# Kernel optimization log

Hardware: AMD Instinct MI355X
Metric: run time of the kernel (lower is better)

## Reference

```python
import jax, jax.numpy as jnp
import numpy as np

H = 512; L = 2; V = 128; B = 128; T = 256; LW = 32; SOS = 1


def _lstm_scan(xs, Wih, Whh, b, reverse=False):
    # xs: [B, T, in]; Wih: [in, 4H]; Whh: [H, 4H]; b: [4H]
    Bq, Hh = xs.shape[0], Whh.shape[0]
    h0 = jnp.zeros((Bq, Hh), xs.dtype)

    def step(carry, xt):
        h, c = carry
        i, f, g, o = jnp.split(xt @ Wih + h @ Whh + b, 4, axis=-1)
        c = jax.nn.sigmoid(f) * c + jax.nn.sigmoid(i) * jnp.tanh(g)
        h = jax.nn.sigmoid(o) * jnp.tanh(c)
        return (h, c), h

    (hT, cT), ys = jax.lax.scan(step, (h0, h0), jnp.swapaxes(xs, 0, 1), reverse=reverse)
    return jnp.swapaxes(ys, 0, 1), hT, cT


def setup_inputs() -> dict:
    key = jax.random.key(0)
    ks = jax.random.split(key, 17)
    s = 0.05
    rn = lambda k, shape: jax.random.normal(k, shape, jnp.float32) * s
    return {
        'x': jax.random.normal(ks[0], (B, T, 2), jnp.float32),
        'enc_l0_Wih': rn(ks[1], (2, 2, 4 * H)),
        'enc_l0_Whh': rn(ks[2], (2, H, 4 * H)),
        'enc_l0_b': rn(ks[3], (2, 4 * H)),
        'enc_l1_Wih': rn(ks[4], (2, 2 * H, 4 * H)),
        'enc_l1_Whh': rn(ks[5], (2, H, 4 * H)),
        'enc_l1_b': rn(ks[6], (2, 4 * H)),
        'dec_Wih': rn(ks[7], (L, H, 4 * H)),
        'dec_Whh': rn(ks[8], (L, H, 4 * H)),
        'dec_b': rn(ks[9], (L, 4 * H)),
        'emb': rn(ks[10], (V, H)),
        'Wq': rn(ks[11], (H, 2 * H)),
        'bq': rn(ks[12], (2 * H,)),
        'Wc': rn(ks[13], (3 * H, H)),
        'bc': rn(ks[14], (H,)),
        'Wf': rn(ks[15], (H, V)),
        'bf': rn(ks[16], (V,)),
    }


def _forward(x, enc_l0_Wih, enc_l0_Whh, enc_l0_b, enc_l1_Wih, enc_l1_Whh, enc_l1_b,
             dec_Wih, dec_Whh, dec_b, emb, Wq, bq, Wc, bc, Wf, bf):
    # --- encoder: 2-layer bidirectional LSTM ---
    hs, cs = [], []
    inp = x
    for (Wih, Whh, b) in ((enc_l0_Wih, enc_l0_Whh, enc_l0_b),
                          (enc_l1_Wih, enc_l1_Whh, enc_l1_b)):
        yf, hf, cf = _lstm_scan(inp, Wih[0], Whh[0], b[0], reverse=False)
        yb, hb, cb = _lstm_scan(inp, Wih[1], Whh[1], b[1], reverse=True)
        inp = jnp.concatenate([yf, yb], axis=-1)
        hs.append(hf + hb)  # sum fwd+bwd final states (as in original)
        cs.append(cf + cb)
    enc_outs = inp                     # [B, T, 2H]
    h0 = jnp.stack(hs)                 # [L, B, H]
    c0 = jnp.stack(cs)
    tok0 = jnp.full((x.shape[0],), SOS, jnp.int32)

    def dec_step(carry, _):
        h, c, tok = carry
        layer_in = emb[tok]            # [B, H]
        nh, nc = [], []
        for l in range(L):
            i, f, g, o = jnp.split(layer_in @ dec_Wih[l] + h[l] @ dec_Whh[l] + dec_b[l], 4, axis=-1)
            cl = jax.nn.sigmoid(f) * c[l] + jax.nn.sigmoid(i) * jnp.tanh(g)
            hl = jax.nn.sigmoid(o) * jnp.tanh(cl)
            nh.append(hl); nc.append(cl)
            layer_in = hl
        dec_out = layer_in             # [B, H]
        query = dec_out @ Wq + bq      # [B, 2H]
        attn = jax.nn.softmax(jnp.einsum('bte,be->bt', enc_outs, query), axis=1)  # [B, T]
        context = jnp.einsum('bt,bte->be', attn, enc_outs)                        # [B, 2H]
        combined = jnp.concatenate([dec_out, context], axis=-1) @ Wc + bc         # [B, H]
        logits = combined @ Wf + bf                                                # [B, V]
        tok = jnp.argmax(logits, axis=-1).astype(jnp.int32)
        return (jnp.stack(nh), jnp.stack(nc), tok), (logits, attn)

    (hF, cF, _), (logits_seq, attn_seq) = jax.lax.scan(dec_step, (h0, c0, tok0), None, length=LW)
    output_seq = jnp.swapaxes(logits_seq, 0, 1)        # [B, LW, V]
    attention = jnp.transpose(attn_seq, (1, 2, 0))     # [B, T, LW]
    return output_seq, hF, cF, attention


def reference(x, enc_l0_Wih, enc_l0_Whh, enc_l0_b, enc_l1_Wih, enc_l1_Whh, enc_l1_b,
              dec_Wih, dec_Whh, dec_b, emb, Wq, bq, Wc, bc, Wf, bf):
    return _forward(x, enc_l0_Wih, enc_l0_Whh, enc_l0_b, enc_l1_Wih, enc_l1_Whh, enc_l1_b,
                    dec_Wih, dec_Whh, dec_b, emb, Wq, bq, Wc, bc, Wf, bf)
```

## Files before the change

### kernel.cpp

```cpp
#include <hip/hip_runtime.h>
#include <hip/hip_fp16.h>
#include <hip/hip_cooperative_groups.h>
#include <math.h>

#define NB 128
#define NT 256
#define NH 512
#define NG 2048
#define NV 128
#define NLW 32

__device__ __forceinline__ float sigf(float x){ return 1.0f/(1.0f + expf(-x)); }
__device__ __forceinline__ void fma4(float4& a, float s, float4 w){
  a.x += s*w.x; a.y += s*w.y; a.z += s*w.z; a.w += s*w.w;
}
__device__ __forceinline__ float4 ldh4(const __half* p){
  const __half2* p2 = (const __half2*)p;
  const float2 a = __half22float2(p2[0]);
  const float2 b = __half22float2(p2[1]);
  return make_float4(a.x, a.y, b.x, b.y);
}
__device__ __forceinline__ void ldh8(const __half* p, float4& lo, float4& hi){
  const float4 raw = *(const float4*)p;
  const __half2* h2 = (const __half2*)&raw;
  const float2 a = __half22float2(h2[0]);
  const float2 b = __half22float2(h2[1]);
  const float2 c = __half22float2(h2[2]);
  const float2 d = __half22float2(h2[3]);
  lo = make_float4(a.x, a.y, b.x, b.y);
  hi = make_float4(c.x, c.y, d.x, d.y);
}
__device__ __forceinline__ void dot4(float& acc, const float4 a, const float4 b){
  acc += a.x*b.x + a.y*b.y + a.z*b.z + a.w*b.w;
}

__device__ __forceinline__ void stc_f(float* p, float v){
  union { float f; unsigned u; } c; c.f = v;
  __hip_atomic_store((unsigned*)p, c.u, __ATOMIC_RELAXED, __HIP_MEMORY_SCOPE_AGENT);
}
__device__ __forceinline__ void stc_i(int* p, int v){
  __hip_atomic_store(p, v, __ATOMIC_RELAXED, __HIP_MEMORY_SCOPE_AGENT);
}

#define BAR_FLAG0 1088
#define BAR_INTS  (1088 + 256*32)

__device__ __forceinline__ void bar_core(int* bar, int step) {
  const int g = blockIdx.x >> 4;
  const int prev = __hip_atomic_fetch_add(&bar[g*64], 1,
                     __ATOMIC_RELAXED, __HIP_MEMORY_SCOPE_AGENT);
  if (prev == 15) {
    const int r = __hip_atomic_fetch_add(&bar[16*64], 1,
                     __ATOMIC_RELAXED, __HIP_MEMORY_SCOPE_AGENT);
    if (r == 15) {
      #pragma unroll
      for (int i = 0; i < 16; ++i)
        __hip_atomic_store(&bar[i*64], 0, __ATOMIC_RELAXED, __HIP_MEMORY_SCOPE_AGENT);
      __hip_atomic_store(&bar[16*64], 0, __ATOMIC_RELAXED, __HIP_MEMORY_SCOPE_AGENT);
      asm volatile("s_waitcnt vmcnt(0)" ::: "memory");
      #pragma unroll 8
      for (int i = 0; i < 256; ++i)
        __hip_atomic_store(&bar[BAR_FLAG0 + i*32], step,
                           __ATOMIC_RELAXED, __HIP_MEMORY_SCOPE_AGENT);
    }
  }
}
__device__ __forceinline__ void grid_arrive(int* bar, int step) {
  __syncthreads();
  if (threadIdx.x == 0) {
    asm volatile("s_waitcnt vmcnt(0)" ::: "memory");
    bar_core(bar, step);
  }
}
__device__ __forceinline__ void grid_arrive_f(int* bar, int step) {
  __syncthreads();
  if (threadIdx.x == 0) {
    __threadfence();
    bar_core(bar, step);
  }
}
__device__ __forceinline__ void grid_wait(int* bar, int step) {
  if (threadIdx.x == 0) {
    int* my = &bar[BAR_FLAG0 + blockIdx.x*32];
    while (__hip_atomic_load(my, __ATOMIC_RELAXED,
                             __HIP_MEMORY_SCOPE_AGENT) < step)
      __builtin_amdgcn_s_sleep(2);
    __threadfence();
  }
  __syncthreads();
}

struct EncParams {
  const float* x;
  const float* W0ih; const float* W0hh; const float* b0;
  const float* W1ih; const float* W1hh; const float* b1;
  __half* y0; __half* enc;
  float* h0buf; float* h1buf;
  float* c0fin; float* c1fin;
  int*   bar;
};

#define W1T_ROW 1542
#define W0T_ROW 518
#define ENC_LDS_FLOATS (16*W1T_ROW + 16*W0T_ROW + 16 + 16 + 128*17)
#define ENC_LDS_BYTES  (ENC_LDS_FLOATS*4)

__device__ __forceinline__ void l1_ih_part(const __half* y0t, const float* W1T,
                                           const float* bias1, int bg2, int cg2,
                                           float acc[2][4]) {
  #pragma unroll
  for (int i = 0; i < 2; ++i)
    #pragma unroll
    for (int j = 0; j < 4; ++j)
      acc[i][j] = bias1[cg2*4 + j];
  const long r0 = (long)(bg2*2+0)*1024, r1 = (long)(bg2*2+1)*1024;
  #pragma unroll 2
  for (int k = 0; k < 1024; k += 8) {
    float4 a0lo, a0hi, a1lo, a1hi;
    ldh8(y0t + r0 + k, a0lo, a0hi);
    ldh8(y0t + r1 + k, a1lo, a1hi);
    #pragma unroll
    for (int j = 0; j < 4; ++j) {
      const float4 wlo = *(const float4*)&W1T[(cg2*4+j)*W1T_ROW + k];
      const float4 whi = *(const float4*)&W1T[(cg2*4+j)*W1T_ROW + k + 4];
      dot4(acc[0][j], a0lo, wlo); dot4(acc[0][j], a0hi, whi);
      dot4(acc[1][j], a1lo, wlo); dot4(acc[1][j], a1hi, whi);
    }
  }
}

__global__ __launch_bounds__(256, 1)
void encoder_kernel(EncParams P) {
  const int tid = threadIdx.x;
  const int bid = blockIdx.x;
  const int dir = bid >> 7;
  const int n0  = (bid & 127) * 4;
  int* bar = P.bar;

  extern __shared__ float lds[];
  float* W1T   = lds;
  float* W0T   = lds + 16*W1T_ROW;
  float* bias0 = W0T + 16*W0T_ROW;
  float* bias1 = bias0 + 16;
  float* gsm   = bias1 + 16;

  {
    const float* Wih1 = P.W1ih + (long)dir*1024*NG;
    const float* Whh1 = P.W1hh + (long)dir*512*NG;
    for (int e = tid; e < 16*1536; e += 256) {
      const int ci = e & 15, kk = e >> 4;
      const int gc = (ci>>2)*NH + n0 + (ci&3);
      W1T[ci*W1T_ROW + kk] = (kk < 1024) ? Wih1[(long)kk*NG + gc]
                                         : Whh1[(long)(kk-1024)*NG + gc];
    }
    const float* Wih0 = P.W0ih + (long)dir*2*NG;
    const float* Whh0 = P.W0hh + (long)dir*512*NG;
    for (int e = tid; e < 16*512; e += 256) {
      const int ci = e & 15, kk = e >> 4;
      const int gc = (ci>>2)*NH + n0 + (ci&3);
      W0T[ci*W0T_ROW + 4 + kk] = Whh0[(long)kk*NG + gc];
    }
    if (tid < 32) {
      const int ci = tid & 15, kk = tid >> 4;
      const int gc = (ci>>2)*NH + n0 + (ci&3);
      W0T[ci*W0T_ROW + kk] = Wih0[(long)kk*NG + gc];
    }
    if (tid < 16) {
      const int gc = (tid>>2)*NH + n0 + (tid&3);
      bias0[tid] = P.b0[(long)dir*NG + gc];
      bias1[tid] = P.b1[(long)dir*NG + gc];
    }
  }
  __syncthreads();

  int gstep = 0;
  float creg0 = 0.f, creg1 = 0.f;

  {
    const int bg1 = tid >> 3;
    const int cg1 = tid & 7;
    for (int p = 0; p < NT; ++p) {
      const int t = dir ? (NT-1 - p) : p;
      const float* hp = P.h0buf + (long)((p&1)*2 + dir)*65536;
      float acc[4][2];
      #pragma unroll
      for (int i = 0; i < 4; ++i) { acc[i][0] = bias0[cg1*2]; acc[i][1] = bias0[cg1*2+1]; }
      {
        const float w00 = W0T[(cg1*2+0)*W0T_ROW + 0], w01 = W0T[(cg1*2+0)*W0T_ROW + 1];
        const float w10 = W0T[(cg1*2+1)*W0T_ROW + 0], w11 = W0T[(cg1*2+1)*W0T_ROW + 1];
        #pragma unroll
        for (int i = 0; i < 4; ++i) {
          const int b = bg1*4 + i;
          const float x0 = P.x[(long)b*(NT*2) + t*2 + 0];
          const float x1 = P.x[(long)b*(NT*2) + t*2 + 1];
          acc[i][0] += x0*w00 + x1*w01;
          acc[i][1] += x0*w10 + x1*w11;
        }
      }
      #pragma unroll 4
      for (int k = 0; k < NH; k += 4) {
        const float4 w0 = *(const float4*)&W0T[(cg1*2+0)*W0T_ROW + 4 + k];
        const float4 w1 = *(const float4*)&W0T[(cg1*2+1)*W0T_ROW + 4 + k];
        #pragma unroll
        for (int i = 0; i < 4; ++i) {
          const float4 a = *(const float4*)&hp[(long)(bg1*4+i)*NH + k];
          dot4(acc[i][0], a, w0);
          dot4(acc[i][1], a, w1);
        }
      }
      #pragma unroll
      for (int i = 0; i < 4; ++i) {
        gsm[(bg1*4+i)*17 + cg1*2 + 0] = acc[i][0];
        gsm[(bg1*4+i)*17 + cg1*2 + 1] = acc[i][1];
      }
      __syncthreads();
      {
        float* hnext = P.h0buf + (long)(((p+1)&1)*2 + dir)*65536;
        #pragma unroll
        for (int r = 0; r < 2; ++r) {
          const int pi2 = tid + r*256;
          const int b = pi2 >> 2, nl = pi2 & 3;
          const float iv = gsm[b*17 + 0  + nl];
          const float fv = gsm[b*17 + 4  + nl];
          const float gv = gsm[b*17 + 8  + nl];
          const float ov = gsm[b*17 + 12 + nl];
          float cold = r ? creg1 : creg0;
          const float cn = sigf(fv)*cold + sigf(iv)*tanhf(gv);
          const float hn = sigf(ov)*tanhf(cn);
          if (r) creg1 = cn; else creg0 = cn;
          stc_f(&hnext[(long)b*NH + n0 + nl], hn);
          P.y0[((long)t*NB + b)*1024 + dir*NH + n0 + nl] = __float2half_rn(hn);
        }
      }
      ++gstep;
      if (p < NT-1) grid_arrive(bar, gstep);
      else          grid_arrive_f(bar, gstep);
      grid_wait(bar, gstep);
    }
    #pragma unroll
    for (int r = 0; r < 2; ++r) {
      const int pi2 = tid + r*256;
      P.c0fin[(long)dir*65536 + (long)(pi2>>2)*NH + n0 + (pi2&3)] = r ? creg1 : creg0;
    }
    creg0 = 0.f; creg1 = 0.f;
  }

  {
    const int bg2 = tid >> 2;
    const int cg2 = tid & 3;
    float accN[2][4], accC[2][4];
    {
      const int t0i = dir ? (NT-1) : 0;
      l1_ih_part(P.y0 + (long)t0i*NB*1024, W1T, bias1, bg2, cg2, accN);
    }
    for (int p = 0; p < NT; ++p) {
      const int t = dir ? (NT-1 - p) : p;
      #pragma unroll
      for (int i = 0; i < 2; ++i)
        #pragma unroll
        for (int j = 0; j < 4; ++j)
          accC[i][j] = accN[i][j];
      {
        const float* hp = P.h1buf + (long)((p&1)*2 + dir)*65536;
        const long r0 = (long)(bg2*2+0)*NH, r1 = (long)(bg2*2+1)*NH;
        #pragma unroll 4
        for (int k = 0; k < NH; k += 4) {
          const float4 w0 = *(const float4*)&W1T[(cg2*4+0)*W1T_ROW + 1024 + k];
          const float4 w1 = *(const float4*)&W1T[(cg2*4+1)*W1T_ROW + 1024 + k];
          const float4 w2 = *(const float4*)&W1T[(cg2*4+2)*W1T_ROW + 1024 + k];
          const float4 w3 = *(const float4*)&W1T[(cg2*4+3)*W1T_ROW + 1024 + k];
          const float4 a0 = *(const float4*)&hp[r0 + k];
          const float4 a1 = *(const float4*)&hp[r1 + k];
          dot4(accC[0][0], a0, w0); dot4(accC[0][1], a0, w1);
          dot4(accC[0][2], a0, w2); dot4(accC[0][3], a0, w3);
          dot4(accC[1][0], a1, w0); dot4(accC[1][1], a1, w1);
          dot4(accC[1][2], a1, w2); dot4(accC[1][3], a1, w3);
        }
      }
      #pragma unroll
      for (int i = 0; i < 2; ++i)
        #pragma unroll
        for (int j = 0; j < 4; ++j)
          gsm[(bg2*2+i)*17 + cg2*4 + j] = accC[i][j];
      __syncthreads();
      {
        float* hnext = P.h1buf + (long)(((p+1)&1)*2 + dir)*65536;
        #pragma unroll
        for (int r = 0; r < 2; ++r) {
          const int pi2 = tid + r*256;
          const int b = pi2 >> 2, nl = pi2 & 3;
          const float iv = gsm[b*17 + 0  + nl];
          const float fv = gsm[b*17 + 4  + nl];
          const float gv = gsm[b*17 + 8  + nl];
          const float ov = gsm[b*17 + 12 + nl];
          float cold = r ? creg1 : creg0;
          const float cn = sigf(fv)*cold + sigf(iv)*tanhf(gv);
          const float hn = sigf(ov)*tanhf(cn);
          if (r) creg1 = cn; else creg0 = cn;
          stc_f(&hnext[(long)b*NH + n0 + nl], hn);
          P.enc[((long)t*NB + b)*1024 + dir*NH + n0 + nl] = __float2half_rn(hn);
        }
      }
      if (p < NT-1) {
        ++gstep; grid_arrive(bar, gstep);
        const int tn = dir ? (NT-1 - (p+1)) : (p+1);
        l1_ih_part(P.y0 + (long)tn*NB*1024, W1T, bias1, bg2, cg2, accN);
        grid_wait(bar, gstep);
      }
    }
    #pragma unroll
    for (int r = 0; r < 2; ++r) {
      const int pi2 = tid + r*256;
      P.c1fin[(long)dir*65536 + (long)(pi2>>2)*NH + n0 + (pi2&3)] = r ? creg1 : creg0;
    }
  }
}

struct DecParams {
  const float* emb;
  const float* dWih; const float* dWhh; const float* dbv;
  const float* Wq;  const float* bq;
  const float* Wc;  const float* bc;
  const float* Wf;  const float* bf;
  const __half* enc;
  const float* h0e; const float* h1e;
  const float* c0fin; const float* c1fin;
  float* dh0; float* dh1;
  float* query; float* ctx; float* comb;
  int*   tok;
  float* dout;
  int*   bar;
};

#define WD_ROW 1026
#define WQ_ROW 514
#define WC_ROW 1538
#define DEC_LDS_FLOATS (16*WD_ROW + 4*WQ_ROW + 2*WC_ROW + 16 + 4 + 2 + 128*17 \
                        + 1024 + 256 + 64 + 4 + 512 + 128 + 128)
#define DEC_LDS_BYTES  (DEC_LDS_FLOATS*4)

__global__ __launch_bounds__(256, 1)
void decoder_kernel(DecParams P) {
  const int tid = threadIdx.x;
  const int lid = blockIdx.x;
  const int L   = lid >> 7;
  const int n0  = (lid & 127) * 4;
  const int qc0 = lid * 4;
  const int cc0 = lid * 2;
  int* bar = P.bar;

  extern __shared__ float lds[];
  float* WD    = lds;
  float* WqT   = WD + 16*WD_ROW;
  float* WcT   = WqT + 4*WQ_ROW;
  float* biasD = WcT + 2*WC_ROW;
  float* bq4   = biasD + 16;
  float* bc2   = bq4 + 4;
  float* gsm   = bc2 + 2;
  float* qs    = gsm + 128*17;
  float* sc    = qs + 1024;
  float* ps    = sc + 256;
  float* m3    = ps + 64;
  float* cs    = m3 + 4;
  float* vals  = cs + 512;
  int*   idxs  = (int*)(vals + 128);

  {
    const float* Wih = P.dWih + (long)L*512*NG;
    const float* Whh = P.dWhh + (long)L*512*NG;
    for (int e = tid; e < 16*1024; e += 256) {
      const int ci = e & 15, kk = e >> 4;
      const int gc = (ci>>2)*NH + n0 + (ci&3);
      WD[ci*WD_ROW + kk] = (kk < 512) ? Wih[(long)kk*NG + gc]
                                      : Whh[(long)(kk-512)*NG + gc];
    }
    for (int e = tid; e < 4*512; e += 256) {
      const int c = e & 3, kk = e >> 2;
      WqT[c*WQ_ROW + kk] = P.Wq[(long)kk*1024 + qc0 + c];
    }
    for (int e = tid; e < 2*1536; e += 256) {
      const int c = e & 1, kk = e >> 1;
      WcT[c*WC_ROW + kk] = P.Wc[(long)kk*NH + cc0 + c];
    }
    if (tid < 16) biasD[tid] = P.dbv[(long)L*NG + (tid>>2)*NH + n0 + (tid&3)];
    if (tid < 4)  bq4[tid] = P.bq[qc0 + tid];
    if (tid < 2)  bc2[tid] = P.bc[cc0 + tid];
    const int i = lid*256 + tid;
    stc_f(&P.dh0[i], P.h0e[i] + P.h0e[65536 + i]);
    stc_f(&P.dh1[i], P.h1e[i] + P.h1e[65536 + i]);
    if (i < NB) stc_i(&P.tok[i], 1);
  }
  float cregA, cregB;
  {
    const float* cf = L ? P.c1fin : P.c0fin;
    const int b0i = tid >> 2, nl0 = tid & 3;
    cregA = cf[(long)b0i*NH + n0 + nl0] + cf[65536 + (long)b0i*NH + n0 + nl0];
    const int pi2 = tid + 256;
    const int b1i = pi2 >> 2, nl1 = pi2 & 3;
    cregB = cf[(long)b1i*NH + n0 + nl1] + cf[65536 + (long)b1i*NH + n0 + nl1];
  }
  int gstep = 0;
  ++gstep; grid_arrive(bar, gstep); grid_wait(bar, gstep);

  const int bg = tid >> 3;
  const int cg = tid & 7;

  for (int s = 0; s < NLW; ++s) {
    float* dh0c = P.dh0 + (s&1)*65536;
    float* dh0n = P.dh0 + ((s+1)&1)*65536;
    float* dh1c = P.dh1 + (s&1)*65536;
    float* dh1n = P.dh1 + ((s+1)&1)*65536;

    if (L == 0) {
      float acc[4][2];
      #pragma unroll
      for (int i = 0; i < 4; ++i) { acc[i][0] = biasD[cg*2]; acc[i][1] = biasD[cg*2+1]; }
      int rows[4];
      #pragma unroll
      for (int i = 0; i < 4; ++i) rows[i] = P.tok[bg*4 + i];
      #pragma unroll 4
      for (int k = 0; k < NH; k += 4) {
        const float4 w0 = *(const float4*)&WD[(cg*2+0)*WD_ROW + k];
        const float4 w1 = *(const float4*)&WD[(cg*2+1)*WD_ROW + k];
        #pragma unroll
        for (int i = 0; i < 4; ++i) {
          const float4 a = *(const float4*)&P.emb[(long)rows[i]*NH + k];
          dot4(acc[i][0], a, w0);
          dot4(acc[i][1], a, w1);
        }
      }
      #pragma unroll 4
      for (int k = 0; k < NH; k += 4) {
        const float4 w0 = *(const float4*)&WD[(cg*2+0)*WD_ROW + 512 + k];
        const float4 w1 = *(const float4*)&WD[(cg*2+1)*WD_ROW + 512 + k];
        #pragma unroll
        for (int i = 0; i < 4; ++i) {
          const float4 a = *(const float4*)&dh0c[(long)(bg*4+i)*NH + k];
          dot4(acc[i][0], a, w0);
          dot4(acc[i][1], a, w1);
        }
      }
      #pragma unroll
      for (int i = 0; i < 4; ++i) {
        gsm[(bg*4+i)*17 + cg*2 + 0] = acc[i][0];
        gsm[(bg*4+i)*17 + cg*2 + 1] = acc[i][1];
      }
      __syncthreads();
      #pragma unroll
      for (int r = 0; r < 2; ++r) {
        const int pi2 = tid + r*256;
        const int b = pi2 >> 2, nl = pi2 & 3;
        const float iv = gsm[b*17 + 0  + nl];
        const float fv = gsm[b*17 + 4  + nl];
        const float gv = gsm[b*17 + 8  + nl];
        const float ov = gsm[b*17 + 12 + nl];
        const float cold = r ? cregB : cregA;
        const float cn = sigf(fv)*cold + sigf(iv)*tanhf(gv);
        const float hn = sigf(ov)*tanhf(cn);
        if (r) cregB = cn; else cregA = cn;
        stc_f(&dh0n[(long)b*NH + n0 + nl], hn);
      }
    }
    ++gstep; grid_arrive(bar, gstep); grid_wait(bar, gstep);

    if (L == 1) {
      float acc[4][2];
      #pragma unroll
      for (int i = 0; i < 4; ++i) { acc[i][0] = biasD[cg*2]; acc[i][1] = biasD[cg*2+1]; }
      #pragma unroll 4
      for (int k = 0; k < NH; k += 4) {
        const float4 w0 = *(const float4*)&WD[(cg*2+0)*WD_ROW + k];
        const float4 w1 = *(const float4*)&WD[(cg*2+1)*WD_ROW + k];
        #pragma unroll
        for (int i = 0; i < 4; ++i) {
          const float4 a = *(const float4*)&dh0n[(long)(bg*4+i)*NH + k];
          dot4(acc[i][0], a, w0);
          dot4(acc[i][1], a, w1);
        }
      }
      #pragma unroll 4
      for (int k = 0; k < NH; k += 4) {
        const float4 w0 = *(const float4*)&WD[(cg*2+0)*WD_ROW + 512 + k];
        const float4 w1 = *(const float4*)&WD[(cg*2+1)*WD_ROW + 512 + k];
        #pragma unroll
        for (int i = 0; i < 4; ++i) {
          const float4 a = *(const float4*)&dh1c[(long)(bg*4+i)*NH + k];
          dot4(acc[i][0], a, w0);
          dot4(acc[i][1], a, w1);
        }
      }
      #pragma unroll
      for (int i = 0; i < 4; ++i) {
        gsm[(bg*4+i)*17 + cg*2 + 0] = acc[i][0];
        gsm[(bg*4+i)*17 + cg*2 + 1] = acc[i][1];
      }
      __syncthreads();
      #pragma unroll
      for (int r = 0; r < 2; ++r) {
        const int pi2 = tid + r*256;
        const int b = pi2 >> 2, nl = pi2 & 3;
        const float iv = gsm[b*17 + 0  + nl];
        const float fv = gsm[b*17 + 4  + nl];
        const float gv = gsm[b*17 + 8  + nl];
        const float ov = gsm[b*17 + 12 + nl];
        const float cold = r ? cregB : cregA;
        const float cn = sigf(fv)*cold + sigf(iv)*tanhf(gv);
        const float hn = sigf(ov)*tanhf(cn);
        if (r) cregB = cn; else cregA = cn;
        stc_f(&dh1n[(long)b*NH + n0 + nl], hn);
      }
    }
    ++gstep; grid_arrive(bar, gstep); grid_wait(bar, gstep);

    {
      const int b = tid >> 1;
      const int ch = (tid & 1) * 2;
      float a0 = bq4[ch + 0], a1 = bq4[ch + 1];
      const float* hr = dh1n + (long)b*NH;
      #pragma unroll 4
      for (int k = 0; k < NH; k += 4) {
        const float4 a = *(const float4*)&hr[k];
        const float4 w0 = *(const float4*)&WqT[(ch+0)*WQ_ROW + k];
        const float4 w1 = *(const float4*)&WqT[(ch+1)*WQ_ROW + k];
        dot4(a0, a, w0);
        dot4(a1, a, w1);
      }
      stc_f(&P.query[(long)b*1024 + qc0 + ch + 0], a0);
      stc_f(&P.query[(long)b*1024 + qc0 + ch + 1], a1);
    }
    ++gstep; grid_arrive(bar, gstep); grid_wait(bar, gstep);

    if (lid < NB) {
      const int b = lid;
      for (int i = tid; i < 1024; i += 256) qs[i] = P.query[(long)b*1024 + i];
      if (tid == 0) { m3[0] = -1e30f; m3[1] = 0.f; m3[2] = 0.f; }
      __syncthreads();
      float4 ctx4 = {0,0,0,0};
      for (int c = 0; c < 4; ++c) {
        const int t0 = c*64;
        {
          const int t_l = tid >> 2, part = tid & 3;
          const __half* er = P.enc + ((long)(t0 + t_l)*NB + b)*1024 + part*256;
          const float* qr = qs + part*256;
          float sv = 0.f;
          for (int k = 0; k < 256; k += 4) {
            const float4 e4 = ldh4(er + k);
            const float4 q4 = *(const float4*)(qr + k);
            sv += e4.x*q4.x + e4.y*q4.y + e4.z*q4.z + e4.w*q4.w;
          }
          sv += __shfl_xor(sv, 1);
          sv += __shfl_xor(sv, 2);
          if (part == 0) sc[t0 + t_l] = sv;
        }
        __syncthreads();
        if (tid < 64) {
          float sv = sc[t0 + tid];
          for (int off = 32; off; off >>= 1) sv = fmaxf(sv, __shfl_xor(sv, off));
          if (tid == 0) {
            const float mn = fmaxf(m3[0], sv);
            m3[2] = expf(m3[0] - mn);
            m3[0] = mn;
          }
        }
        __syncthreads();
        const float alpha = m3[2];
        if (tid < 64) {
          float pv = expf(sc[t0 + tid] - m3[0]);
          ps[tid] = pv;
          for (int off = 32; off; off >>= 1) pv += __shfl_xor(pv, off);
          if (tid == 0) m3[1] = m3[1]*alpha + pv;
        }
        __syncthreads();
        ctx4.x *= alpha; ctx4.y *= alpha; ctx4.z *= alpha; ctx4.w *= alpha;
        const __half* ecol = P.enc + ((long)t0*NB + b)*1024 + tid*4;
        for (int t = 0; t < 64; ++t) {
          const float4 e4 = ldh4(ecol + (long)t*(NB*1024));
          fma4(ctx4, ps[t], e4);
        }
        __syncthreads();
      }
      const float linv = 1.0f / m3[1];
      const long cb = (long)b*1024 + tid*4;
      stc_f(&P.ctx[cb+0], ctx4.x*linv); stc_f(&P.ctx[cb+1], ctx4.y*linv);
      stc_f(&P.ctx[cb+2], ctx4.z*linv); stc_f(&P.ctx[cb+3], ctx4.w*linv);
      const float pv = expf(sc[tid] - m3[0]) * linv;
      stc_f(&P.dout[786432L + (long)b*(NT*NLW) + (long)tid*NLW + s], pv);
    }
    ++gstep; grid_arrive(bar, gstep); grid_wait(bar, gstep);

    {
      const int b = tid >> 1;
      const int col = tid & 1;
      float acc = bc2[col];
      const float* hr = dh1n + (long)b*NH;
      #pragma unroll 4
      for (int k = 0; k < NH; k += 4) {
        const float4 a = *(const float4*)&hr[k];
        const float4 w = *(const float4*)&WcT[col*WC_ROW + k];
        dot4(acc, a, w);
      }
      const float* cr = P.ctx + (long)b*1024;
      #pragma unroll 4
      for (int k = 0; k < 1024; k += 4) {
        const float4 a = *(const float4*)&cr[k];
        const float4 w = *(const float4*)&WcT[col*WC_ROW + 512 + k];
        dot4(acc, a, w);
      }
      stc_f(&P.comb[(long)b*NH + cc0 + col], acc);
    }
    ++gstep; grid_arrive(bar, gstep); grid_wait(bar, gstep);

    if (lid < NB) {
      const int b = lid;
      for (int i = tid; i < NH; i += 256) cs[i] = P.comb[(long)b*NH + i];
      __syncthreads();
      if (tid < NV) {
        float acc = P.bf[tid];
        for (int k = 0; k < NH; k += 4) {
          const float4 c4 = *(const float4*)&cs[k];
          acc += c4.x*P.Wf[(long)(k+0)*NV + tid];
          acc += c4.y*P.Wf[(long)(k+1)*NV + tid];
          acc += c4.z*P.Wf[(long)(k+2)*NV + tid];
          acc += c4.w*P.Wf[(long)(k+3)*NV + tid];
        }
        stc_f(&P.dout[(long)b*(NLW*NV) + (long)s*NV + tid], acc);
        vals[tid] = acc; idxs[tid] = tid;
      }
      __syncthreads();
      for (int st = 64; st > 0; st >>= 1) {
        if (tid < st) {
          const float v2 = vals[tid+st]; const int i2 = idxs[tid+st];
          if (v2 > vals[tid] || (v2 == vals[tid] && i2 < idxs[tid])) { vals[tid] = v2; idxs[tid] = i2; }
        }
        __syncthreads();
      }
      if (tid == 0) stc_i(&P.tok[b], idxs[0]);
    }
    ++gstep; grid_arrive(bar, gstep); grid_wait(bar, gstep);
  }

  {
    const int i = lid*256 + tid;
    P.dout[524288L + i]         = P.dh0[i];
    P.dout[524288L + 65536 + i] = P.dh1[i];
    #pragma unroll
    for (int r = 0; r < 2; ++r) {
      const int pi2 = tid + r*256;
      const int b = pi2 >> 2, nl = pi2 & 3;
      P.dout[655360L + (long)L*65536 + (long)b*NH + n0 + nl] = r ? cregB : cregA;
    }
  }
}

struct StepDir {
  const void*  A;
  const float* WA;
  const float* Bs;
  const float* WB;
  const float* x2;
  const float* Wx;
  const int*   rowIdxA;
  const float* bias;
  float*  c_io;
  float*  h_out;
  __half* yh_out;
  int sA, KA, sB, KB, sx2, ystride, aHalf;
};
struct StepParams { StepDir d[2]; };

__global__ __launch_bounds__(256)
void lstm_step_kernel(StepParams P) {
  const StepDir p = P.d[blockIdx.z];
  const int tid = threadIdx.x;
  const int nq  = tid & 3;
  const int g   = (tid >> 2) & 3;
  const int bp  = tid >> 4;
  const int bl0 = bp*2;
  const int b0  = blockIdx.y*32 + bl0;
  const int n0  = blockIdx.x*16 + nq*4;
  const int gc  = g*NH + n0;

  float4 acc0 = *(const float4*)(p.bias + gc);
  float4 acc1 = acc0;

  if (p.x2) {
    const float4 w0 = *(const float4*)(p.Wx + gc);
    const float4 w1 = *(const float4*)(p.Wx + NG + gc);
    const float* xr0 = p.x2 + (long)b0     * p.sx2;
    const float* xr1 = p.x2 + (long)(b0+1) * p.sx2;
    fma4(acc0, xr0[0], w0); fma4(acc0, xr0[1], w1);
    fma4(acc1, xr1[0], w0); fma4(acc1, xr1[1], w1);
  }
  if (p.KA > 0) {
    const int r0 = p.rowIdxA ? p.rowIdxA[b0]   : b0;
    const int r1 = p.rowIdxA ? p.rowIdxA[b0+1] : b0+1;
    const float* Wp = p.WA + gc;
    if (p.aHalf) {
      const __half* rA0 = (const __half*)p.A + (long)r0 * p.sA;
      const __half* rA1 = (const __half*)p.A + (long)r1 * p.sA;
      for (int k = 0; k < p.KA; k += 4) {
        const float4 a0 = ldh4(rA0 + k);
        const float4 a1 = ldh4(rA1 + k);
        const float4 w0 = *(const float4*)(Wp + (long)(k+0)*NG);
        const float4 w1 = *(const float4*)(Wp + (long)(k+1)*NG);
        const float4 w2 = *(const float4*)(Wp + (long)(k+2)*NG);
        const float4 w3 = *(const float4*)(Wp + (long)(k+3)*NG);
        fma4(acc0, a0.x, w0); fma4(acc0, a0.y, w1); fma4(acc0, a0.z, w2); fma4(acc0, a0.w, w3);
        fma4(acc1, a1.x, w0); fma4(acc1, a1.y, w1); fma4(acc1, a1.z, w2); fma4(acc1, a1.w, w3);
      }
    } else {
      const float* rA0 = (const float*)p.A + (long)r0 * p.sA;
      const float* rA1 = (const float*)p.A + (long)r1 * p.sA;
      for (int k = 0; k < p.KA; k += 4) {
        const float4 a0 = *(const float4*)(rA0 + k);
        const float4 a1 = *(const float4*)(rA1 + k);
        const float4 w0 = *(const float4*)(Wp + (long)(k+0)*NG);
        const float4 w1 = *(const float4*)(Wp + (long)(k+1)*NG);
        const float4 w2 = *(const float4*)(Wp + (long)(k+2)*NG);
        const float4 w3 = *(const float4*)(Wp + (long)(k+3)*NG);
        fma4(acc0, a0.x, w0); fma4(acc0, a0.y, w1); fma4(acc0, a0.z, w2); fma4(acc0, a0.w, w3);
        fma4(acc1, a1.x, w0); fma4(acc1, a1.y, w1); fma4(acc1, a1.z, w2); fma4(acc1, a1.w, w3);
      }
    }
  }
  {
    const float* rB0 = p.Bs + (long)b0     * p.sB;
    const float* rB1 = p.Bs + (long)(b0+1) * p.sB;
    const float* Wp = p.WB + gc;
    for (int k = 0; k < p.KB; k += 4) {
      const float4 a0 = *(const float4*)(rB0 + k);
      const float4 a1 = *(const float4*)(rB1 + k);
      const float4 w0 = *(const float4*)(Wp + (long)(k+0)*NG);
      const float4 w1 = *(const float4*)(Wp + (long)(k+1)*NG);
      const float4 w2 = *(const float4*)(Wp + (long)(k+2)*NG);
      const float4 w3 = *(const float4*)(Wp + (long)(k+3)*NG);
      fma4(acc0, a0.x, w0); fma4(acc0, a0.y, w1); fma4(acc0, a0.z, w2); fma4(acc0, a0.w, w3);
      fma4(acc1, a1.x, w0); fma4(acc1, a1.y, w1); fma4(acc1, a1.z, w2); fma4(acc1, a1.w, w3);
    }
  }

  __shared__ __align__(16) float gs[32][68];
  {
    float* r0 = &gs[bl0][g*17 + nq*4];
    r0[0]=acc0.x; r0[1]=acc0.y; r0[2]=acc0.z; r0[3]=acc0.w;
    float* r1 = &gs[bl0+1][g*17 + nq*4];
    r1[0]=acc1.x; r1[1]=acc1.y; r1[2]=acc1.z; r1[3]=acc1.w;
  }
  __syncthreads();
  for (int pi = tid; pi < 512; pi += 256) {
    const int b_l = pi >> 4, n_l = pi & 15;
    const float iv = gs[b_l][0*17 + n_l];
    const float fv = gs[b_l][1*17 + n_l];
    const float gv = gs[b_l][2*17 + n_l];
    const float ov = gs[b_l][3*17 + n_l];
    const int bg = blockIdx.y*32 + b_l;
    const long idx = (long)bg*NH + blockIdx.x*16 + n_l;
    const float c_old = p.c_io[idx];
    const float cn = sigf(fv)*c_old + sigf(iv)*tanhf(gv);
    const float hn = sigf(ov)*tanhf(cn);
    p.c_io[idx]  = cn;
    p.h_out[idx] = hn;
    if (p.yh_out)
      p.yh_out[(long)bg*p.ystride + blockIdx.x*16 + n_l] = __float2half_rn(hn);
  }
}

struct LinParams {
  const float* A; const float* Bs; const float* W; const float* bias;
  float* out;
  int sA, KA, sB, KB, N;
};

__global__ __launch_bounds__(256)
void linear2_kernel(LinParams p) {
  __shared__ __align__(16) float As[64][36];
  const int tid = threadIdx.x;
  const int jl = tid & 63;
  const int j = blockIdx.x*64 + jl;
  const int bo = (tid >> 6)*8;
  const int bbase = blockIdx.y*32;
  float acc[8] = {0,0,0,0,0,0,0,0};
  for (int src = 0; src < 2; ++src) {
    const float* A = src ? p.Bs : p.A;
    const int sA   = src ? p.sB : p.sA;
    const int K    = src ? p.KB : p.KA;
    const float* W = src ? (p.W + (long)p.KA*p.N) : p.W;
    if (!A || K <= 0) continue;
    for (int k0 = 0; k0 < K; k0 += 64) {
      __syncthreads();
      for (int e = tid; e < 32*64; e += 256) {
        const int bl = e >> 6, kk = e & 63;
        As[kk][bl] = A[(long)(bbase+bl)*sA + k0 + kk];
      }
      __syncthreads();
      const float* Wp = W + (long)k0*p.N + j;
      for (int k = 0; k < 64; ++k) {
        const float wv = Wp[(long)k*p.N];
        const float4 aA = *(const float4*)&As[k][bo];
        const float4 aB = *(const float4*)&As[k][bo+4];
        acc[0] += aA.x*wv; acc[1] += aA.y*wv; acc[2] += aA.z*wv; acc[3] += aA.w*wv;
        acc[4] += aB.x*wv; acc[5] += aB.y*wv; acc[6] += aB.z*wv; acc[7] += aB.w*wv;
      }
    }
  }
  const float bv = p.bias ? p.bias[j] : 0.f;
  for (int i = 0; i < 8; ++i)
    p.out[(long)(bbase + bo + i)*p.N + j] = acc[i] + bv;
}

__global__ __launch_bounds__(256)
void attn_kernel(const float* __restrict__ query, const __half* __restrict__ enc,
                 float* __restrict__ context, float* __restrict__ attn_out, int step) {
  const int b = blockIdx.x;
  const int tid = threadIdx.x;
  __shared__ __align__(16) float qs[1024];
  __shared__ float sc[256];
  __shared__ float ps[64];
  __shared__ float msh, lsh, ash;
  for (int i = tid; i < 1024; i += 256) qs[i] = query[(long)b*1024 + i];
  if (tid == 0) { msh = -1e30f; lsh = 0.f; ash = 0.f; }
  __syncthreads();
  float4 ctx = {0,0,0,0};
  for (int c = 0; c < 4; ++c) {
    const int t0 = c*64;
    {
      const int t_l = tid >> 2, part = tid & 3;
      const __half* er = enc + ((long)(t0 + t_l)*NB + b)*1024 + part*256;
      const float* qr = qs + part*256;
      float sv = 0.f;
      for (int k = 0; k < 256; k += 4) {
        const float4 e4 = ldh4(er + k);
        const float4 q4 = *(const float4*)(qr + k);
        sv += e4.x*q4.x + e4.y*q4.y + e4.z*q4.z + e4.w*q4.w;
      }
      sv += __shfl_xor(sv, 1);
      sv += __shfl_xor(sv, 2);
      if (part == 0) sc[t0 + t_l] = sv;
    }
    __syncthreads();
    if (tid < 64) {
      float sv = sc[t0 + tid];
      for (int off = 32; off; off >>= 1) sv = fmaxf(sv, __shfl_xor(sv, off));
      if (tid == 0) {
        const float mn = fmaxf(msh, sv);
        ash = expf(msh - mn);
        msh = mn;
      }
    }
    __syncthreads();
    const float alpha = ash;
    if (tid < 64) {
      float pv = expf(sc[t0 + tid] - msh);
      ps[tid] = pv;
      for (int off = 32; off; off >>= 1) pv += __shfl_xor(pv, off);
      if (tid == 0) lsh = lsh*alpha + pv;
    }
    __syncthreads();
    ctx.x *= alpha; ctx.y *= alpha; ctx.z *= alpha; ctx.w *= alpha;
    const __half* ecol = enc + ((long)t0*NB + b)*1024 + tid*4;
    for (int t = 0; t < 64; ++t) {
      const float4 e4 = ldh4(ecol + (long)t*(NB*1024));
      fma4(ctx, ps[t], e4);
    }
    __syncthreads();
  }
  const float linv = 1.0f / lsh;
  const long cb = (long)b*1024 + tid*4;
  context[cb+0] = ctx.x*linv; context[cb+1] = ctx.y*linv;
  context[cb+2] = ctx.z*linv; context[cb+3] = ctx.w*linv;
  const float pv = expf(sc[tid] - msh) * linv;
  attn_out[(long)b*(NT*NLW) + (long)tid*NLW + step] = pv;
}

__global__ __launch_bounds__(128)
void logits_kernel(const float* __restrict__ comb, const float* __restrict__ Wf,
                   const float* __restrict__ bfv, float* __restrict__ out,
                   int sOut, int* __restrict__ tok) {
  const int b = blockIdx.x;
  const int v = threadIdx.x;
  __shared__ __align__(16) float cs[512];
  __shared__ float vals[128];
  __shared__ int idxs[128];
  for (int i = v; i < 512; i += 128) cs[i] = comb[(long)b*512 + i];
  __syncthreads();
  float acc = bfv[v];
  for (int k = 0; k < 512; k += 4) {
    const float4 c4 = *(const float4*)&cs[k];
    acc += c4.x*Wf[(long)(k+0)*NV + v];
    acc += c4.y*Wf[(long)(k+1)*NV + v];
    acc += c4.z*Wf[(long)(k+2)*NV + v];
    acc += c4.w*Wf[(long)(k+3)*NV + v];
  }
  out[(long)b*sOut + v] = acc;
  vals[v] = acc; idxs[v] = v;
  __syncthreads();
  for (int s = 64; s > 0; s >>= 1) {
    if (v < s) {
      const float v2 = vals[v+s]; const int i2 = idxs[v+s];
      if (v2 > vals[v] || (v2 == vals[v] && i2 < idxs[v])) { vals[v] = v2; idxs[v] = i2; }
    }
    __syncthreads();
  }
  if (v == 0) tok[b] = idxs[0];
}

__global__ void init_dec_kernel(const float* h00, const float* h01,
                                const float* c00, const float* c01,
                                const float* h10, const float* h11,
                                const float* c10, const float* c11,
                                float* dh0, float* dh1, float* dc0, float* dc1,
                                int* tok) {
  const int i = blockIdx.x*256 + threadIdx.x;
  dh0[i] = h00[i] + h01[i];
  dc0[i] = c00[i] + c01[i];
  dh1[i] = h10[i] + h11[i];
  dc1[i] = c10[i] + c11[i];
  if (i < NB) tok[i] = 1;
}

__global__ void final_copy_kernel(const float* dh0, const float* dh1,
                                  const float* dc0, const float* dc1,
                                  float* out_h, float* out_c) {
  const int i = blockIdx.x*256 + threadIdx.x;
  out_h[i] = dh0[i]; out_h[65536 + i] = dh1[i];
  out_c[i] = dc0[i]; out_c[65536 + i] = dc1[i];
}

extern "C" void kernel_launch(void* const* d_in, const int* in_sizes, int n_in,
                              void* d_out_v, int out_size, void* d_ws, size_t ws_size,
                              hipStream_t stream) {
  (void)in_sizes; (void)n_in; (void)out_size;
  const float* x    = (const float*)d_in[0];
  const float* W0ih = (const float*)d_in[1];
  const float* W0hh = (const float*)d_in[2];
  const float* b0v  = (const float*)d_in[3];
  const float* W1ih = (const float*)d_in[4];
  const float* W1hh = (const float*)d_in[5];
  const float* b1v  = (const float*)d_in[6];
  const float* dWih = (const float*)d_in[7];
  const float* dWhh = (const float*)d_in[8];
  const float* dbv  = (const float*)d_in[9];
  const float* emb  = (const float*)d_in[10];
  const float* Wq   = (const float*)d_in[11];
  const float* bq   = (const float*)d_in[12];
  const float* Wc   = (const float*)d_in[13];
  const float* bc   = (const float*)d_in[14];
  const float* Wf   = (const float*)d_in[15];
  const float* bfv  = (const float*)d_in[16];

  const long Y0_SLOTS  = 16777216L;
  const long ENC_SLOTS = 16777216L;
  const long BAR_SLOTS = 2L*9472;
  const long ST_SZ     = 786432L + BAR_SLOTS;
  const long DEC_SZ    = 655488L;
  const long NEEDED    = Y0_SLOTS + ENC_SLOTS + ST_SZ + DEC_SZ;
  if (ws_size < (size_t)NEEDED*4) return;

  float*  ws    = (float*)d_ws;
  __half* y0h   = (__half*)ws;
  __half* ench  = (__half*)(ws + Y0_SLOTS);
  float*  st    = ws + Y0_SLOTS + ENC_SLOTS;
  float*  h0buf = st;
  float*  h1buf = st + 262144;
  float*  c0fin = st + 524288;
  float*  c1fin = st + 655360;
  int*    barE  = (int*)(st + 786432);
  int*    barD  = barE + 9472;
  float*  dec   = st + ST_SZ;
  float* ddh0  = dec + 0;
  float* ddh1  = dec + 131072;
  float* dcomb = dec + 262144;
  float* query = dec + 393216;
  float* ctx   = dec + 524288;
  int*   tok   = (int*)(dec + 655360);
  float* dh[2][2] = {{dec+0, dec+65536}, {dec+131072, dec+196608}};
  float* dc[2]    =  {dec+262144, dec+327680};
  float* comb  = query;
  float* dout  = (float*)d_out_v;

  hipMemsetAsync(st, 0, ST_SZ*4, stream);

  EncParams EP;
  EP.x = x; EP.W0ih = W0ih; EP.W0hh = W0hh; EP.b0 = b0v;
  EP.W1ih = W1ih; EP.W1hh = W1hh; EP.b1 = b1v;
  EP.y0 = y0h; EP.enc = ench;
  EP.h0buf = h0buf; EP.h1buf = h1buf; EP.c0fin = c0fin; EP.c1fin = c1fin;
  EP.bar = barE;

  static int attrDone = 0;
  if (!attrDone) {
    (void)hipFuncSetAttribute(reinterpret_cast<const void*>(encoder_kernel),
                              hipFuncAttributeMaxDynamicSharedMemorySize,
                              ENC_LDS_BYTES);
    (void)hipFuncSetAttribute(reinterpret_cast<const void*>(decoder_kernel),
                              hipFuncAttributeMaxDynamicSharedMemorySize,
                              DEC_LDS_BYTES);
    attrDone = 1;
  }
  void* eargs[] = { (void*)&EP };
  hipError_t cerr = hipLaunchCooperativeKernel(
      reinterpret_cast<const void*>(encoder_kernel),
      dim3(256), dim3(256), eargs, (unsigned int)ENC_LDS_BYTES, stream);

  if (cerr != hipSuccess) {
    for (int p = 0; p < NT; ++p) {
      StepParams SP{};
      for (int d = 0; d < 2; ++d) {
        const int t = d ? (NT-1-p) : p;
        StepDir& q = SP.d[d];
        q.A = nullptr; q.WA = nullptr; q.sA = 0; q.KA = 0; q.aHalf = 0;
        q.Bs = h0buf + (long)((p&1)*2 + d)*65536; q.sB = NH; q.KB = NH;
        q.WB = W0hh + (long)d*NH*NG;
        q.x2 = x + (long)t*2; q.sx2 = NT*2; q.Wx = W0ih + (long)d*2*NG;
        q.rowIdxA = nullptr; q.bias = b0v + (long)d*NG;
        q.c_io = c0fin + (long)d*65536;
        q.h_out = h0buf + (long)(((p+1)&1)*2 + d)*65536;
        q.yh_out = y0h + (long)t*(NB*1024) + d*NH; q.ystride = 1024;
      }
      lstm_step_kernel<<<dim3(32,4,2), 256, 0, stream>>>(SP);
    }
    for (int p = 0; p < NT; ++p) {
      StepParams SP{};
      for (int d = 0; d < 2; ++d) {
        const int t = d ? (NT-1-p) : p;
        StepDir& q = SP.d[d];
        q.A = y0h + (long)t*(NB*1024); q.aHalf = 1; q.sA = 1024; q.KA = 2*NH;
        q.WA = W1ih + (long)d*(2*NH)*NG;
        q.Bs = h1buf + (long)((p&1)*2 + d)*65536; q.sB = NH; q.KB = NH;
        q.WB = W1hh + (long)d*NH*NG;
        q.x2 = nullptr; q.sx2 = 0; q.Wx = nullptr;
        q.rowIdxA = nullptr; q.bias = b1v + (long)d*NG;
        q.c_io = c1fin + (long)d*65536;
        q.h_out = h1buf + (long)(((p+1)&1)*2 + d)*65536;
        q.yh_out = ench + (long)t*(NB*1024) + d*NH; q.ystride = 1024;
      }
      lstm_step_kernel<<<dim3(32,4,2), 256, 0, stream>>>(SP);
    }
  }

  DecParams DP;
  DP.emb = emb; DP.dWih = dWih; DP.dWhh = dWhh; DP.dbv = dbv;
  DP.Wq = Wq; DP.bq = bq; DP.Wc = Wc; DP.bc = bc; DP.Wf = Wf; DP.bf = bfv;
  DP.enc = ench;
  DP.h0e = h0buf; DP.h1e = h1buf;
  DP.c0fin = c0fin; DP.c1fin = c1fin;
  DP.dh0 = ddh0; DP.dh1 = ddh1;
  DP.query = query; DP.ctx = ctx; DP.comb = dcomb;
  DP.tok = tok; DP.dout = dout; DP.bar = barD;

  void* dargs[] = { (void*)&DP };
  hipError_t derr = hipLaunchCooperativeKernel(
      reinterpret_cast<const void*>(decoder_kernel),
      dim3(256), dim3(256), dargs, (unsigned int)DEC_LDS_BYTES, stream);

  if (derr != hipSuccess) {
    init_dec_kernel<<<256, 256, 0, stream>>>(h0buf, h0buf+65536, c0fin, c0fin+65536,
                                             h1buf, h1buf+65536, c1fin, c1fin+65536,
                                             dh[0][0], dh[1][0], dc[0], dc[1], tok);
    for (int s = 0; s < NLW; ++s) {
      const int si = s&1, so = (s+1)&1;
      {
        StepParams SP{};
        StepDir& q = SP.d[0];
        q.A = emb; q.sA = NH; q.KA = NH; q.aHalf = 0; q.WA = dWih;
        q.Bs = dh[0][si]; q.sB = NH; q.KB = NH; q.WB = dWhh;
        q.x2 = nullptr; q.sx2 = 0; q.Wx = nullptr;
        q.rowIdxA = tok;
        q.bias = dbv;
        q.c_io = dc[0]; q.h_out = dh[0][so];
        q.yh_out = nullptr; q.ystride = 0;
        lstm_step_kernel<<<dim3(32,4,1), 256, 0, stream>>>(SP);
      }
      {
        StepParams SP{};
        StepDir& q = SP.d[0];
        q.A = dh[0][so]; q.sA = NH; q.KA = NH; q.aHalf = 0; q.WA = dWih + (long)NH*NG;
        q.Bs = dh[1][si]; q.sB = NH; q.KB = NH; q.WB = dWhh + (long)NH*NG;
        q.x2 = nullptr; q.sx2 = 0; q.Wx = nullptr;
        q.rowIdxA = nullptr;
        q.bias = dbv + NG;
        q.c_io = dc[1]; q.h_out = dh[1][so];
        q.yh_out = nullptr; q.ystride = 0;
        lstm_step_kernel<<<dim3(32,4,1), 256, 0, stream>>>(SP);
      }
      {
        LinParams LP{ dh[1][so], nullptr, Wq, bq, query, NH, NH, 0, 0, 2*NH };
        linear2_kernel<<<dim3(16,4), 256, 0, stream>>>(LP);
      }
      attn_kernel<<<128, 256, 0, stream>>>(query, ench, ctx, dout + 786432L, s);
      {
        LinParams LP{ dh[1][so], ctx, Wc, bc, comb, NH, NH, 2*NH, 2*NH, NH };
        linear2_kernel<<<dim3(8,4), 256, 0, stream>>>(LP);
      }
      logits_kernel<<<128, 128, 0, stream>>>(comb, Wf, bfv, dout + (long)s*NV,
                                             NLW*NV, tok);
    }
    final_copy_kernel<<<256, 256, 0, stream>>>(dh[0][0], dh[1][0], dc[0], dc[1],
                                               dout + 524288L, dout + 655360L);
  }
}
```

Before: 39.45 ms.

## Split encoder grid barrier into per-direction barriers for independent fwd/bwd LSTMs

```diff
diff --git a/kernel.cpp b/kernel.cpp
--- a/kernel.cpp
+++ b/kernel.cpp
@@ -42,10 +42,10 @@
   __hip_atomic_store(p, v, __ATOMIC_RELAXED, __HIP_MEMORY_SCOPE_AGENT);
 }
 
-#define BAR_FLAG0 1088
-#define BAR_INTS  (1088 + 256*32)
-
-__device__ __forceinline__ void bar_core(int* bar, int step) {
+#define FBAR_FLAG0 1088
+#define DBAR_FLAG0 1024
+
+__device__ __forceinline__ void full_core(int* bar, int step) {
   const int g = blockIdx.x >> 4;
   const int prev = __hip_atomic_fetch_add(&bar[g*64], 1,
                      __ATOMIC_RELAXED, __HIP_MEMORY_SCOPE_AGENT);
@@ -60,28 +60,64 @@
       asm volatile("s_waitcnt vmcnt(0)" ::: "memory");
       #pragma unroll 8
       for (int i = 0; i < 256; ++i)
-        __hip_atomic_store(&bar[BAR_FLAG0 + i*32], step,
+        __hip_atomic_store(&bar[FBAR_FLAG0 + i*32], step,
                            __ATOMIC_RELAXED, __HIP_MEMORY_SCOPE_AGENT);
     }
   }
 }
-__device__ __forceinline__ void grid_arrive(int* bar, int step) {
+__device__ __forceinline__ void full_arrive(int* bar, int step) {
   __syncthreads();
   if (threadIdx.x == 0) {
     asm volatile("s_waitcnt vmcnt(0)" ::: "memory");
-    bar_core(bar, step);
-  }
-}
-__device__ __forceinline__ void grid_arrive_f(int* bar, int step) {
+    full_core(bar, step);
+  }
+}
+__device__ __forceinline__ void full_arrive_f(int* bar, int step) {
   __syncthreads();
   if (threadIdx.x == 0) {
     __threadfence();
-    bar_core(bar, step);
-  }
-}
-__device__ __forceinline__ void grid_wait(int* bar, int step) {
+    full_core(bar, step);
+  }
+}
+__device__ __forceinline__ void full_wait(int* bar, int step) {
   if (threadIdx.x == 0) {
-    int* my = &bar[BAR_FLAG0 + blockIdx.x*32];
+    int* my = &bar[FBAR_FLAG0 + blockIdx.x*32];
+    while (__hip_atomic_load(my, __ATOMIC_RELAXED,
+                             __HIP_MEMORY_SCOPE_AGENT) < step)
+      __builtin_amdgcn_s_sleep(2);
+    __threadfence();
+  }
+  __syncthreads();
+}
+
+__device__ __forceinline__ void dir_arrive(int* dbar, int step) {
+  __syncthreads();
+  if (threadIdx.x == 0) {
+    asm volatile("s_waitcnt vmcnt(0)" ::: "memory");
+    const int l = blockIdx.x & 127;
+    const int g = l >> 4;
+    const int prev = __hip_atomic_fetch_add(&dbar[g*64], 1,
+                       __ATOMIC_RELAXED, __HIP_MEMORY_SCOPE_AGENT);
+    if (prev == 15) {
+      const int r = __hip_atomic_fetch_add(&dbar[8*64], 1,
+                       __ATOMIC_RELAXED, __HIP_MEMORY_SCOPE_AGENT);
+      if (r == 7) {
+        #pragma unroll
+        for (int i = 0; i < 8; ++i)
+          __hip_atomic_store(&dbar[i*64], 0, __ATOMIC_RELAXED, __HIP_MEMORY_SCOPE_AGENT);
+        __hip_atomic_store(&dbar[8*64], 0, __ATOMIC_RELAXED, __HIP_MEMORY_SCOPE_AGENT);
+        asm volatile("s_waitcnt vmcnt(0)" ::: "memory");
+        #pragma unroll 8
+        for (int i = 0; i < 128; ++i)
+          __hip_atomic_store(&dbar[DBAR_FLAG0 + i*32], step,
+                             __ATOMIC_RELAXED, __HIP_MEMORY_SCOPE_AGENT);
+      }
+    }
+  }
+}
+__device__ __forceinline__ void dir_wait(int* dbar, int step) {
+  if (threadIdx.x == 0) {
+    int* my = &dbar[DBAR_FLAG0 + (blockIdx.x & 127)*32];
     while (__hip_atomic_load(my, __ATOMIC_RELAXED,
                              __HIP_MEMORY_SCOPE_AGENT) < step)
       __builtin_amdgcn_s_sleep(2);
@@ -135,7 +171,8 @@
   const int bid = blockIdx.x;
   const int dir = bid >> 7;
   const int n0  = (bid & 127) * 4;
-  int* bar = P.bar;
+  int* dbar = P.bar + dir*8192;
+  int* fbar = P.bar + 16384;
 
   extern __shared__ float lds[];
   float* W1T   = lds;
@@ -173,7 +210,7 @@
   }
   __syncthreads();
 
-  int gstep = 0;
+  int dstep = 0;
   float creg0 = 0.f, creg1 = 0.f;
 
   {
@@ -232,10 +269,8 @@
           P.y0[((long)t*NB + b)*1024 + dir*NH + n0 + nl] = __float2half_rn(hn);
         }
       }
-      ++gstep;
-      if (p < NT-1) grid_arrive(bar, gstep);
-      else          grid_arrive_f(bar, gstep);
-      grid_wait(bar, gstep);
+      if (p < NT-1) { ++dstep; dir_arrive(dbar, dstep); dir_wait(dbar, dstep); }
+      else          { full_arrive_f(fbar, 1); full_wait(fbar, 1); }
     }
     #pragma unroll
     for (int r = 0; r < 2; ++r) {
@@ -302,10 +337,10 @@
         }
       }
       if (p < NT-1) {
-        ++gstep; grid_arrive(bar, gstep);
+        ++dstep; dir_arrive(dbar, dstep);
         const int tn = dir ? (NT-1 - (p+1)) : (p+1);
         l1_ih_part(P.y0 + (long)tn*NB*1024, W1T, bias1, bg2, cg2, accN);
-        grid_wait(bar, gstep);
+        dir_wait(dbar, dstep);
       }
     }
     #pragma unroll
@@ -400,7 +435,7 @@
     cregB = cf[(long)b1i*NH + n0 + nl1] + cf[65536 + (long)b1i*NH + n0 + nl1];
   }
   int gstep = 0;
-  ++gstep; grid_arrive(bar, gstep); grid_wait(bar, gstep);
+  ++gstep; full_arrive(bar, gstep); full_wait(bar, gstep);
 
   const int bg = tid >> 3;
   const int cg = tid & 7;
@@ -461,7 +496,7 @@
         stc_f(&dh0n[(long)b*NH + n0 + nl], hn);
       }
     }
-    ++gstep; grid_arrive(bar, gstep); grid_wait(bar, gstep);
+    ++gstep; full_arrive(bar, gstep); full_wait(bar, gstep);
 
     if (L == 1) {
       float acc[4][2];
@@ -510,7 +545,7 @@
         stc_f(&dh1n[(long)b*NH + n0 + nl], hn);
       }
     }
-    ++gstep; grid_arrive(bar, gstep); grid_wait(bar, gstep);
+    ++gstep; full_arrive(bar, gstep); full_wait(bar, gstep);
 
     {
       const int b = tid >> 1;
@@ -528,7 +563,7 @@
       stc_f(&P.query[(long)b*1024 + qc0 + ch + 0], a0);
       stc_f(&P.query[(long)b*1024 + qc0 + ch + 1], a1);
     }
-    ++gstep; grid_arrive(bar, gstep); grid_wait(bar, gstep);
+    ++gstep; full_arrive(bar, gstep); full_wait(bar, gstep);
 
     if (lid < NB) {
       const int b = lid;
@@ -586,7 +621,7 @@
       const float pv = expf(sc[tid] - m3[0]) * linv;
       stc_f(&P.dout[786432L + (long)b*(NT*NLW) + (long)tid*NLW + s], pv);
     }
-    ++gstep; grid_arrive(bar, gstep); grid_wait(bar, gstep);
+    ++gstep; full_arrive(bar, gstep); full_wait(bar, gstep);
 
     {
       const int b = tid >> 1;
@@ -608,7 +643,7 @@
       }
       stc_f(&P.comb[(long)b*NH + cc0 + col], acc);
     }
-    ++gstep; grid_arrive(bar, gstep); grid_wait(bar, gstep);
+    ++gstep; full_arrive(bar, gstep); full_wait(bar, gstep);
 
     if (lid < NB) {
       const int b = lid;
@@ -636,7 +671,7 @@
       }
       if (tid == 0) stc_i(&P.tok[b], idxs[0]);
     }
-    ++gstep; grid_arrive(bar, gstep); grid_wait(bar, gstep);
+    ++gstep; full_arrive(bar, gstep); full_wait(bar, gstep);
   }
 
   {
@@ -950,7 +985,7 @@
 
   const long Y0_SLOTS  = 16777216L;
   const long ENC_SLOTS = 16777216L;
-  const long BAR_SLOTS = 2L*9472;
+  const long BAR_SLOTS = 40960L;
   const long ST_SZ     = 786432L + BAR_SLOTS;
   const long DEC_SZ    = 655488L;
   const long NEEDED    = Y0_SLOTS + ENC_SLOTS + ST_SZ + DEC_SZ;
@@ -965,7 +1000,7 @@
   float*  c0fin = st + 524288;
   float*  c1fin = st + 655360;
   int*    barE  = (int*)(st + 786432);
-  int*    barD  = barE + 9472;
+  int*    barD  = barE + 28672;
   float*  dec   = st + ST_SZ;
   float* ddh0  = dec + 0;
   float* ddh1  = dec + 131072;
```

New measurement: 39.66 ms. Within noise of the previous version (+0.5%).
